# Kernel tuning notes

Hardware: AMD Instinct MI355X
Metric: run time of the kernel (lower is better)

Reference implementation:

```python
import jax, jax.numpy as jnp
import numpy as np

N_NODES = 50000
N_EDGES = 25000  # hyperedges
NNZ = 400000     # incidence pairs


def _segment_mean(x, idx, num_segments):
    s = jax.ops.segment_sum(x, idx, num_segments=num_segments)
    cnt = jax.ops.segment_sum(jnp.ones((x.shape[0], 1), x.dtype), idx, num_segments=num_segments)
    return s / jnp.maximum(cnt, 1.0)


def _unigcn_conv(X, W, vertex, edges, degE, degV):
    # X: [N, Cin] -> [N, Cout]
    X = X @ W                                   # linear (no bias)
    Xve = X[vertex]                             # gather per incidence [nnz, C]
    Xe = _segment_mean(Xve, edges, N_EDGES)     # first_aggregate='mean' over hyperedges
    Xe = Xe * degE                              # [M,1] scale
    Xev = Xe[edges]                             # gather back [nnz, C]
    Xv = jax.ops.segment_sum(Xev, vertex, num_segments=N_NODES)
    return Xv * degV                            # [N,1] scale


def setup_inputs() -> dict:
    key = jax.random.key(0)
    ks = jax.random.split(key, 8)
    nfeat, nhid_total, nclass = 512, 512, 40
    def glorot(k, fan_in, fan_out):
        std = np.sqrt(6.0 / (fan_in + fan_out))
        return jax.random.uniform(k, (fan_in, fan_out), jnp.float32, -std, std)
    return {
        "X": jax.random.normal(ks[0], (N_NODES, nfeat), jnp.float32),
        "vertex": jax.random.randint(ks[1], (NNZ,), 0, N_NODES, jnp.int32),
        "edges": jax.random.randint(ks[2], (NNZ,), 0, N_EDGES, jnp.int32),
        "W1": glorot(ks[3], nfeat, nhid_total),
        "W2": glorot(ks[4], nhid_total, nhid_total),
        "Wout": glorot(ks[5], nhid_total, nclass),
        "degE": jax.random.uniform(ks[6], (N_EDGES, 1), jnp.float32, 0.1, 1.0),
        "degV": jax.random.uniform(ks[7], (N_NODES, 1), jnp.float32, 0.1, 1.0),
    }


def reference(X, vertex, edges, W1, W2, Wout, degE, degV):
    # dropout layers are identity at eval (rates = 0)
    X = jax.nn.relu(_unigcn_conv(X, W1, vertex, edges, degE, degV))
    X = jax.nn.relu(_unigcn_conv(X, W2, vertex, edges, degE, degV))
    X = _unigcn_conv(X, Wout, vertex, edges, degE, degV)
    return jax.nn.log_softmax(X, axis=1)
```

## Files before the change

### kernel.cpp

```cpp
#include <hip/hip_runtime.h>

#define N_NODES 50000
#define N_EDGES_C 25000
#define NNZ_C 400000
#define SCHUNK 2048

typedef __bf16 bf16;
typedef __bf16 bf16x8 __attribute__((ext_vector_type(8)));
typedef __bf16 bf16x4 __attribute__((ext_vector_type(4)));
typedef float f32x4 __attribute__((ext_vector_type(4)));

typedef __attribute__((address_space(1))) const void as1_cvoid;
typedef __attribute__((address_space(3))) void as3_void;

__device__ __forceinline__ void gload_lds16(const bf16* g, bf16* l) {
  __builtin_amdgcn_global_load_lds((as1_cvoid*)g, (as3_void*)l, 16, 0, 0);
}

__global__ void hist_kernel(const int* __restrict__ vtx, const int* __restrict__ edg,
                            int* __restrict__ cntV, int* __restrict__ cntE, int nnz) {
  int i = blockIdx.x * blockDim.x + threadIdx.x;
  if (i < nnz) {
    atomicAdd(&cntV[vtx[i]], 1);
    atomicAdd(&cntE[edg[i]], 1);
  }
}

__global__ void scan_part(const int* __restrict__ cnt, int* __restrict__ part, int n) {
  __shared__ int red[256];
  const int b = blockIdx.x, t = threadIdx.x;
  const int base = b * SCHUNK + t * 8;
  int s = 0;
#pragma unroll
  for (int q = 0; q < 8; ++q) {
    int i = base + q;
    if (i < n) s += cnt[i];
  }
  red[t] = s;
  __syncthreads();
  for (int d = 128; d > 0; d >>= 1) {
    if (t < d) red[t] += red[t + d];
    __syncthreads();
  }
  if (t == 0) part[b] = red[0];
}

__global__ void scan_mid(int* __restrict__ part, int* __restrict__ off, int nparts, int n) {
  const int lane = threadIdx.x;
  int orig = (lane < nparts) ? part[lane] : 0;
  int v = orig;
  for (int o = 1; o < 64; o <<= 1) {
    int x = __shfl_up(v, o);
    if (lane >= o) v += x;
  }
  if (lane < nparts) part[lane] = v - orig;
  if (lane == 63) off[n] = v;
}

__global__ void scan_final(const int* __restrict__ cnt, const int* __restrict__ part,
                           int* __restrict__ off, int n) {
  __shared__ int tsum[256];
  const int b = blockIdx.x, t = threadIdx.x;
  const int base = b * SCHUNK + t * 8;
  int loc[8];
  int s = 0;
#pragma unroll
  for (int q = 0; q < 8; ++q) {
    int i = base + q;
    loc[q] = (i < n) ? cnt[i] : 0;
    s += loc[q];
  }
  tsum[t] = s;
  __syncthreads();
  for (int d = 1; d < 256; d <<= 1) {
    int x = (t >= d) ? tsum[t - d] : 0;
    __syncthreads();
    tsum[t] += x;
    __syncthreads();
  }
  int run = part[b] + ((t > 0) ? tsum[t - 1] : 0);
#pragma unroll
  for (int q = 0; q < 8; ++q) {
    int i = base + q;
    if (i < n) off[i] = run;
    run += loc[q];
  }
}

__global__ void scatter_kernel(const int* __restrict__ vtx, const int* __restrict__ edg,
                               const int* __restrict__ eoff, const int* __restrict__ voff,
                               int* __restrict__ curE, int* __restrict__ curV,
                               int* __restrict__ evtx, int* __restrict__ vedg, int nnz) {
  int i = blockIdx.x * blockDim.x + threadIdx.x;
  if (i < nnz) {
    int e = edg[i], v = vtx[i];
    int p = atomicAdd(&curE[e], 1);
    evtx[eoff[e] + p] = v;
    int q = atomicAdd(&curV[v], 1);
    vedg[voff[v] + q] = e;
  }
}

__global__ void convert_f2b(const float* __restrict__ in, bf16* __restrict__ out, size_t n) {
  size_t i = ((size_t)blockIdx.x * blockDim.x + threadIdx.x) * 4;
  if (i >= n) return;
  float4 v = *(const float4*)(in + i);
  bf16x4 o;
  o[0] = (bf16)v.x; o[1] = (bf16)v.y; o[2] = (bf16)v.z; o[3] = (bf16)v.w;
  *(bf16x4*)(out + i) = o;
}

__global__ void transpose_w(const float* __restrict__ W, bf16* __restrict__ Wt,
                            int K, int N, int NtRows) {
  int idx = blockIdx.x * blockDim.x + threadIdx.x;
  int total = NtRows * K;
  if (idx >= total) return;
  int n = idx / K;
  int k = idx - n * K;
  Wt[idx] = (n < N) ? (bf16)W[(size_t)k * N + n] : (bf16)0.0f;
}

template <int BF16OUT>
__global__ __launch_bounds__(256) void gemm_bf16_kernel(
    const bf16* __restrict__ A, const bf16* __restrict__ B,
    float* __restrict__ Cf, bf16* __restrict__ Cb, int M, int K, int ldC, int Nstore) {
  __shared__ bf16 Al[2][128][64];
  __shared__ bf16 Bl[2][128][64];
  const int t = threadIdx.x;
  const int m0 = blockIdx.x * 128;
  const int n0 = blockIdx.y * 128;
  const int w = t >> 6, lane = t & 63;
  const int wr = w >> 1, wc = w & 1;
  const int lr = lane & 15;
  const int ls = lane >> 4;

  f32x4 acc[4][4];
#pragma unroll
  for (int m = 0; m < 4; ++m)
#pragma unroll
    for (int n = 0; n < 4; ++n) acc[m][n] = (f32x4){0.f, 0.f, 0.f, 0.f};

  const int srow8 = lane >> 3;
  const int scol = ((lane & 7) ^ srow8) << 3;

  const bf16* Abase = A + (size_t)m0 * K;
  const bf16* Bbase = B + (size_t)n0 * K;

#define STAGE(tile, bsel)                                                        \
  {                                                                              \
    const int kk_ = (tile) * 64;                                                 \
    _Pragma("unroll")                                                            \
    for (int q = 0; q < 4; ++q) {                                                \
      const int row = w * 32 + q * 8 + srow8;                                    \
      gload_lds16(Abase + (size_t)row * K + kk_ + scol, &Al[bsel][w*32+q*8][0]); \
      gload_lds16(Bbase + (size_t)row * K + kk_ + scol, &Bl[bsel][w*32+q*8][0]); \
    }                                                                            \
  }

  const int NT = K >> 6;
  STAGE(0, 0);
  for (int tt = 0; tt < NT; ++tt) {
    const int cur = tt & 1;
    if (tt + 1 < NT) {
      STAGE(tt + 1, cur ^ 1);
      asm volatile("s_waitcnt vmcnt(8)" ::: "memory");
    } else {
      asm volatile("s_waitcnt vmcnt(0)" ::: "memory");
    }
    __builtin_amdgcn_s_barrier();
    __builtin_amdgcn_s_setprio(1);
#pragma unroll
    for (int ks = 0; ks < 2; ++ks) {
      bf16x8 af[4], bfr[4];
#pragma unroll
      for (int m = 0; m < 4; ++m) {
        const int R = wr * 64 + m * 16 + lr;
        af[m] = *(const bf16x8*)(&Al[cur][R][((ks * 4 + ls) ^ (lr & 7)) << 3]);
      }
#pragma unroll
      for (int n = 0; n < 4; ++n) {
        const int R = wc * 64 + n * 16 + lr;
        bfr[n] = *(const bf16x8*)(&Bl[cur][R][((ks * 4 + ls) ^ (lr & 7)) << 3]);
      }
#pragma unroll
      for (int m = 0; m < 4; ++m)
#pragma unroll
        for (int n = 0; n < 4; ++n)
          acc[m][n] = __builtin_amdgcn_mfma_f32_16x16x32_bf16(af[m], bfr[n], acc[m][n], 0, 0, 0);
    }
    __builtin_amdgcn_s_setprio(0);
    __builtin_amdgcn_s_barrier();
  }
#undef STAGE

  const int cr = (lane >> 4) << 2;
  const int cc = lane & 15;
#pragma unroll
  for (int m = 0; m < 4; ++m) {
#pragma unroll
    for (int n = 0; n < 4; ++n) {
      int gc = n0 + wc * 64 + n * 16 + cc;
      if (gc >= Nstore) continue;
#pragma unroll
      for (int i = 0; i < 4; ++i) {
        int gr = m0 + wr * 64 + m * 16 + cr + i;
        if (gr < M) {
          if (BF16OUT) Cb[(size_t)gr * ldC + gc] = (bf16)acc[m][n][i];
          else         Cf[(size_t)gr * ldC + gc] = acc[m][n][i];
        }
      }
    }
  }
}

__global__ __launch_bounds__(256) void edge_agg_w(
    const bf16* __restrict__ Y, const int* __restrict__ eoff, const int* __restrict__ evtx,
    const float* __restrict__ degE, bf16* __restrict__ Xe, int nE) {
  const int wv = (blockIdx.x * 256 + threadIdx.x) >> 6;
  if (wv >= nE) return;
  const int lane = threadIdx.x & 63;
  const int beg = eoff[wv], end = eoff[wv + 1];
  const int cnt = end - beg;
  const float scale = (cnt > 0) ? degE[wv] / (float)cnt : 0.f;
  float acc[8] = {0.f, 0.f, 0.f, 0.f, 0.f, 0.f, 0.f, 0.f};
  for (int base = beg; base < end; base += 64) {
    const int nb = min(64, end - base);
    int myidx = (lane < nb) ? evtx[base + lane] : 0;
    int j = 0;
    for (; j + 1 < nb; j += 2) {
      const int i0 = __shfl(myidx, j);
      const int i1 = __shfl(myidx, j + 1);
      bf16x8 v0 = *(const bf16x8*)(Y + (size_t)i0 * 512 + lane * 8);
      bf16x8 v1 = *(const bf16x8*)(Y + (size_t)i1 * 512 + lane * 8);
#pragma unroll
      for (int q = 0; q < 8; ++q) acc[q] += (float)v0[q] + (float)v1[q];
    }
    if (j < nb) {
      const int i0 = __shfl(myidx, j);
      bf16x8 v0 = *(const bf16x8*)(Y + (size_t)i0 * 512 + lane * 8);
#pragma unroll
      for (int q = 0; q < 8; ++q) acc[q] += (float)v0[q];
    }
  }
  bf16x8 o;
#pragma unroll
  for (int q = 0; q < 8; ++q) o[q] = (bf16)(acc[q] * scale);
  *(bf16x8*)(Xe + (size_t)wv * 512 + lane * 8) = o;
}

__global__ __launch_bounds__(256) void vtx_agg_w(
    const bf16* __restrict__ Xe, const int* __restrict__ voff, const int* __restrict__ vedg,
    const float* __restrict__ degV, bf16* __restrict__ outB, int nV) {
  const int wv = (blockIdx.x * 256 + threadIdx.x) >> 6;
  if (wv >= nV) return;
  const int lane = threadIdx.x & 63;
  const int beg = voff[wv], end = voff[wv + 1];
  const float dv = degV[wv];
  float acc[8] = {0.f, 0.f, 0.f, 0.f, 0.f, 0.f, 0.f, 0.f};
  for (int base = beg; base < end; base += 64) {
    const int nb = min(64, end - base);
    int myidx = (lane < nb) ? vedg[base + lane] : 0;
    int j = 0;
    for (; j + 1 < nb; j += 2) {
      const int i0 = __shfl(myidx, j);
      const int i1 = __shfl(myidx, j + 1);
      bf16x8 v0 = *(const bf16x8*)(Xe + (size_t)i0 * 512 + lane * 8);
      bf16x8 v1 = *(const bf16x8*)(Xe + (size_t)i1 * 512 + lane * 8);
#pragma unroll
      for (int q = 0; q < 8; ++q) acc[q] += (float)v0[q] + (float)v1[q];
    }
    if (j < nb) {
      const int i0 = __shfl(myidx, j);
      bf16x8 v0 = *(const bf16x8*)(Xe + (size_t)i0 * 512 + lane * 8);
#pragma unroll
      for (int q = 0; q < 8; ++q) acc[q] += (float)v0[q];
    }
  }
  bf16x8 o;
#pragma unroll
  for (int q = 0; q < 8; ++q) o[q] = (bf16)fmaxf(acc[q] * dv, 0.f);
  *(bf16x8*)(outB + (size_t)wv * 512 + lane * 8) = o;
}

__global__ __launch_bounds__(256) void edge_agg40_w(
    const float* __restrict__ Y, const int* __restrict__ eoff, const int* __restrict__ evtx,
    const float* __restrict__ degE, float* __restrict__ Xe, int nE) {
  const int wv = (blockIdx.x * 256 + threadIdx.x) >> 6;
  if (wv >= nE) return;
  const int lane = threadIdx.x & 63;
  const int beg = eoff[wv], end = eoff[wv + 1];
  const int cnt = end - beg;
  const float scale = (cnt > 0) ? degE[wv] / (float)cnt : 0.f;
  float a0 = 0.f;
  for (int base = beg; base < end; base += 64) {
    const int nb = min(64, end - base);
    int myidx = (lane < nb) ? evtx[base + lane] : 0;
    int j = 0;
    for (; j + 3 < nb; j += 4) {
      const int i0 = __shfl(myidx, j);
      const int i1 = __shfl(myidx, j + 1);
      const int i2 = __shfl(myidx, j + 2);
      const int i3 = __shfl(myidx, j + 3);
      if (lane < 40) {
        float x0 = Y[(size_t)i0 * 40 + lane];
        float x1 = Y[(size_t)i1 * 40 + lane];
        float x2 = Y[(size_t)i2 * 40 + lane];
        float x3 = Y[(size_t)i3 * 40 + lane];
        a0 += (x0 + x1) + (x2 + x3);
      }
    }
    for (; j < nb; ++j) {
      const int i0 = __shfl(myidx, j);
      if (lane < 40) a0 += Y[(size_t)i0 * 40 + lane];
    }
  }
  if (lane < 40) Xe[(size_t)wv * 40 + lane] = a0 * scale;
}

__global__ __launch_bounds__(256) void vtx_agg_lsm(
    const float* __restrict__ Xe, const int* __restrict__ voff, const int* __restrict__ vedg,
    const float* __restrict__ degV, float* __restrict__ out, int nV) {
  const int wv = (blockIdx.x * 256 + threadIdx.x) >> 6;
  if (wv >= nV) return;
  const int lane = threadIdx.x & 63;
  const int beg = voff[wv], end = voff[wv + 1];
  const float dv = degV[wv];
  float a0 = 0.f;
  for (int base = beg; base < end; base += 64) {
    const int nb = min(64, end - base);
    int myidx = (lane < nb) ? vedg[base + lane] : 0;
    int j = 0;
    for (; j + 3 < nb; j += 4) {
      const int i0 = __shfl(myidx, j);
      const int i1 = __shfl(myidx, j + 1);
      const int i2 = __shfl(myidx, j + 2);
      const int i3 = __shfl(myidx, j + 3);
      if (lane < 40) {
        float x0 = Xe[(size_t)i0 * 40 + lane];
        float x1 = Xe[(size_t)i1 * 40 + lane];
        float x2 = Xe[(size_t)i2 * 40 + lane];
        float x3 = Xe[(size_t)i3 * 40 + lane];
        a0 += (x0 + x1) + (x2 + x3);
      }
    }
    for (; j < nb; ++j) {
      const int i0 = __shfl(myidx, j);
      if (lane < 40) a0 += Xe[(size_t)i0 * 40 + lane];
    }
  }
  a0 *= dv;
  float val = (lane < 40) ? a0 : -3.4e38f;
  float m = val;
#pragma unroll
  for (int o = 32; o > 0; o >>= 1) m = fmaxf(m, __shfl_xor(m, o));
  float ex = (lane < 40) ? expf(val - m) : 0.f;
  float s = ex;
#pragma unroll
  for (int o = 32; o > 0; o >>= 1) s += __shfl_xor(s, o);
  float ls = logf(s);
  if (lane < 40) out[(size_t)wv * 40 + lane] = val - m - ls;
}

extern "C" void kernel_launch(void* const* d_in, const int* in_sizes, int n_in,
                              void* d_out, int out_size, void* d_ws, size_t ws_size,
                              hipStream_t stream) {
  (void)in_sizes; (void)n_in; (void)out_size; (void)ws_size;
  const float* X = (const float*)d_in[0];
  const int* vertex = (const int*)d_in[1];
  const int* edges = (const int*)d_in[2];
  const float* W1 = (const float*)d_in[3];
  const float* W2 = (const float*)d_in[4];
  const float* Wout = (const float*)d_in[5];
  const float* degE = (const float*)d_in[6];
  const float* degV = (const float*)d_in[7];
  float* out = (float*)d_out;

  char* ws = (char*)d_ws;
  size_t off = 0;
  auto alloc = [&](size_t bytes) -> void* {
    void* p = ws + off;
    off += (bytes + 255) & ~(size_t)255;
    return p;
  };
  bf16* Xb  = (bf16*)alloc((size_t)N_NODES * 512 * sizeof(bf16));
  bf16* Yb  = (bf16*)alloc((size_t)N_NODES * 512 * sizeof(bf16));
  bf16* XeB = (bf16*)alloc((size_t)N_EDGES_C * 512 * sizeof(bf16));
  float* Y40  = (float*)alloc((size_t)N_NODES * 40 * sizeof(float));
  float* Xe40 = (float*)alloc((size_t)N_EDGES_C * 40 * sizeof(float));
  bf16* Wt  = (bf16*)alloc((size_t)512 * 512 * sizeof(bf16));
  int* eoff = (int*)alloc((N_EDGES_C + 1) * sizeof(int));
  int* voff = (int*)alloc((N_NODES + 1) * sizeof(int));
  int* evtx = (int*)alloc((size_t)NNZ_C * sizeof(int));
  int* vedg = (int*)alloc((size_t)NNZ_C * sizeof(int));
  int* cntE = (int*)alloc(N_EDGES_C * sizeof(int));
  int* cntV = (int*)alloc(N_NODES * sizeof(int));
  int* curE = (int*)alloc(N_EDGES_C * sizeof(int));
  int* curV = (int*)alloc(N_NODES * sizeof(int));
  int* partE = (int*)alloc(64 * sizeof(int));
  int* partV = (int*)alloc(64 * sizeof(int));

  hipMemsetAsync(cntE, 0, N_EDGES_C * sizeof(int), stream);
  hipMemsetAsync(cntV, 0, N_NODES * sizeof(int), stream);
  hipMemsetAsync(curE, 0, N_EDGES_C * sizeof(int), stream);
  hipMemsetAsync(curV, 0, N_NODES * sizeof(int), stream);

  hist_kernel<<<(NNZ_C + 255) / 256, 256, 0, stream>>>(vertex, edges, cntV, cntE, NNZ_C);

  const int nbE = (N_EDGES_C + SCHUNK - 1) / SCHUNK;
  const int nbV = (N_NODES + SCHUNK - 1) / SCHUNK;
  scan_part<<<nbE, 256, 0, stream>>>(cntE, partE, N_EDGES_C);
  scan_mid<<<1, 64, 0, stream>>>(partE, eoff, nbE, N_EDGES_C);
  scan_final<<<nbE, 256, 0, stream>>>(cntE, partE, eoff, N_EDGES_C);
  scan_part<<<nbV, 256, 0, stream>>>(cntV, partV, N_NODES);
  scan_mid<<<1, 64, 0, stream>>>(partV, voff, nbV, N_NODES);
  scan_final<<<nbV, 256, 0, stream>>>(cntV, partV, voff, N_NODES);

  scatter_kernel<<<(NNZ_C + 255) / 256, 256, 0, stream>>>(vertex, edges, eoff, voff,
                                                          curE, curV, evtx, vedg, NNZ_C);

  convert_f2b<<<(N_NODES * 512 / 4 + 255) / 256, 256, 0, stream>>>(X, Xb, (size_t)N_NODES * 512);

  const int MB = (N_NODES + 127) / 128;

  transpose_w<<<(512 * 512 + 255) / 256, 256, 0, stream>>>(W1, Wt, 512, 512, 512);
  {
    dim3 g(MB, 4);
    gemm_bf16_kernel<1><<<g, 256, 0, stream>>>(Xb, Wt, nullptr, Yb, N_NODES, 512, 512, 512);
  }
  edge_agg_w<<<(N_EDGES_C + 3) / 4, 256, 0, stream>>>(Yb, eoff, evtx, degE, XeB, N_EDGES_C);
  vtx_agg_w<<<(N_NODES + 3) / 4, 256, 0, stream>>>(XeB, voff, vedg, degV, Xb, N_NODES);

  transpose_w<<<(512 * 512 + 255) / 256, 256, 0, stream>>>(W2, Wt, 512, 512, 512);
  {
    dim3 g(MB, 4);
    gemm_bf16_kernel<1><<<g, 256, 0, stream>>>(Xb, Wt, nullptr, Yb, N_NODES, 512, 512, 512);
  }
  edge_agg_w<<<(N_EDGES_C + 3) / 4, 256, 0, stream>>>(Yb, eoff, evtx, degE, XeB, N_EDGES_C);
  vtx_agg_w<<<(N_NODES + 3) / 4, 256, 0, stream>>>(XeB, voff, vedg, degV, Xb, N_NODES);

  transpose_w<<<(128 * 512 + 255) / 256, 256, 0, stream>>>(Wout, Wt, 512, 40, 128);
  {
    dim3 g(MB, 1);
    gemm_bf16_kernel<0><<<g, 256, 0, stream>>>(Xb, Wt, Y40, nullptr, N_NODES, 512, 40, 40);
  }
  edge_agg40_w<<<(N_EDGES_C + 3) / 4, 256, 0, stream>>>(Y40, eoff, evtx, degE, Xe40, N_EDGES_C);
  vtx_agg_lsm<<<(N_NODES + 3) / 4, 256, 0, stream>>>(Xe40, voff, vedg, degV, out, N_NODES);
}
```

Measured before the change: 543.7 us.

## Merge prep and scan launches, swap GEMM grid order, store final layer in bf16

Fuses the weight transposes and the X conversion into one prep kernel, and merges the paired E/V scan kernels and the four memsets into single launches to cut launch count. The GEMM grid is reordered so the four N-tiles of the same M rows run next to each other, which should improve L2 reuse of A. The 40-wide final layer now stores its intermediates in bf16, halving gather traffic at some precision cost.

```diff
diff --git a/kernel.cpp b/kernel.cpp
--- a/kernel.cpp
+++ b/kernel.cpp
@@ -26,9 +26,15 @@
   }
 }
 
-__global__ void scan_part(const int* __restrict__ cnt, int* __restrict__ part, int n) {
+__global__ void scan_part2(const int* __restrict__ cntE, const int* __restrict__ cntV,
+                           int* __restrict__ partE, int* __restrict__ partV,
+                           int nbE) {
   __shared__ int red[256];
-  const int b = blockIdx.x, t = threadIdx.x;
+  const int t = threadIdx.x;
+  const int isV = (blockIdx.x >= nbE);
+  const int b = isV ? (blockIdx.x - nbE) : blockIdx.x;
+  const int* cnt = isV ? cntV : cntE;
+  const int n = isV ? N_NODES : N_EDGES_C;
   const int base = b * SCHUNK + t * 8;
   int s = 0;
 #pragma unroll
@@ -42,25 +48,39 @@
     if (t < d) red[t] += red[t + d];
     __syncthreads();
   }
-  if (t == 0) part[b] = red[0];
-}
-
-__global__ void scan_mid(int* __restrict__ part, int* __restrict__ off, int nparts, int n) {
-  const int lane = threadIdx.x;
-  int orig = (lane < nparts) ? part[lane] : 0;
+  if (t == 0) (isV ? partV : partE)[b] = red[0];
+}
+
+__global__ void scan_mid2(int* __restrict__ partE, int* __restrict__ partV,
+                          int* __restrict__ eoff, int* __restrict__ voff,
+                          int nbE, int nbV) {
+  const int wv = threadIdx.x >> 6;
+  const int lane = threadIdx.x & 63;
+  int* part = wv ? partV : partE;
+  int* off = wv ? voff : eoff;
+  const int np = wv ? nbV : nbE;
+  const int n = wv ? N_NODES : N_EDGES_C;
+  int orig = (lane < np) ? part[lane] : 0;
   int v = orig;
   for (int o = 1; o < 64; o <<= 1) {
     int x = __shfl_up(v, o);
     if (lane >= o) v += x;
   }
-  if (lane < nparts) part[lane] = v - orig;
+  if (lane < np) part[lane] = v - orig;
   if (lane == 63) off[n] = v;
 }
 
-__global__ void scan_final(const int* __restrict__ cnt, const int* __restrict__ part,
-                           int* __restrict__ off, int n) {
+__global__ void scan_final2(const int* __restrict__ cntE, const int* __restrict__ cntV,
+                            const int* __restrict__ partE, const int* __restrict__ partV,
+                            int* __restrict__ eoff, int* __restrict__ voff, int nbE) {
   __shared__ int tsum[256];
-  const int b = blockIdx.x, t = threadIdx.x;
+  const int t = threadIdx.x;
+  const int isV = (blockIdx.x >= nbE);
+  const int b = isV ? (blockIdx.x - nbE) : blockIdx.x;
+  const int* cnt = isV ? cntV : cntE;
+  const int* part = isV ? partV : partE;
+  int* off = isV ? voff : eoff;
+  const int n = isV ? N_NODES : N_EDGES_C;
   const int base = b * SCHUNK + t * 8;
   int loc[8];
   int s = 0;
@@ -101,23 +121,33 @@
   }
 }
 
-__global__ void convert_f2b(const float* __restrict__ in, bf16* __restrict__ out, size_t n) {
-  size_t i = ((size_t)blockIdx.x * blockDim.x + threadIdx.x) * 4;
-  if (i >= n) return;
-  float4 v = *(const float4*)(in + i);
-  bf16x4 o;
-  o[0] = (bf16)v.x; o[1] = (bf16)v.y; o[2] = (bf16)v.z; o[3] = (bf16)v.w;
-  *(bf16x4*)(out + i) = o;
-}
-
-__global__ void transpose_w(const float* __restrict__ W, bf16* __restrict__ Wt,
-                            int K, int N, int NtRows) {
-  int idx = blockIdx.x * blockDim.x + threadIdx.x;
-  int total = NtRows * K;
-  if (idx >= total) return;
-  int n = idx / K;
-  int k = idx - n * K;
-  Wt[idx] = (n < N) ? (bf16)W[(size_t)k * N + n] : (bf16)0.0f;
+__global__ void prep_conv(const float* __restrict__ W1, const float* __restrict__ W2,
+                          const float* __restrict__ Wout, const float* __restrict__ X,
+                          bf16* __restrict__ Wt1, bf16* __restrict__ Wt2,
+                          bf16* __restrict__ Wt3, bf16* __restrict__ Xb) {
+  const int b = blockIdx.x;
+  const int t = threadIdx.x;
+  if (b < 1024) {
+    int idx = b * 256 + t;
+    int n = idx >> 9, k = idx & 511;
+    Wt1[idx] = (bf16)W1[(size_t)k * 512 + n];
+  } else if (b < 2048) {
+    int idx = (b - 1024) * 256 + t;
+    int n = idx >> 9, k = idx & 511;
+    Wt2[idx] = (bf16)W2[(size_t)k * 512 + n];
+  } else if (b < 2304) {
+    int idx = (b - 2048) * 256 + t;
+    int n = idx >> 9, k = idx & 511;
+    Wt3[idx] = (n < 40) ? (bf16)Wout[(size_t)k * 40 + n] : (bf16)0.0f;
+  } else {
+    size_t i = ((size_t)(b - 2304) * 256 + t) * 8;
+    float4 v0 = *(const float4*)(X + i);
+    float4 v1 = *(const float4*)(X + i + 4);
+    bf16x8 o;
+    o[0] = (bf16)v0.x; o[1] = (bf16)v0.y; o[2] = (bf16)v0.z; o[3] = (bf16)v0.w;
+    o[4] = (bf16)v1.x; o[5] = (bf16)v1.y; o[6] = (bf16)v1.z; o[7] = (bf16)v1.w;
+    *(bf16x8*)(Xb + i) = o;
+  }
 }
 
 template <int BF16OUT>
@@ -127,8 +157,8 @@
   __shared__ bf16 Al[2][128][64];
   __shared__ bf16 Bl[2][128][64];
   const int t = threadIdx.x;
-  const int m0 = blockIdx.x * 128;
-  const int n0 = blockIdx.y * 128;
+  const int n0 = blockIdx.x * 128;
+  const int m0 = blockIdx.y * 128;
   const int w = t >> 6, lane = t & 63;
   const int wr = w >> 1, wc = w & 1;
   const int lr = lane & 15;
@@ -283,8 +313,8 @@
 }
 
 __global__ __launch_bounds__(256) void edge_agg40_w(
-    const float* __restrict__ Y, const int* __restrict__ eoff, const int* __restrict__ evtx,
-    const float* __restrict__ degE, float* __restrict__ Xe, int nE) {
+    const bf16* __restrict__ Y, const int* __restrict__ eoff, const int* __restrict__ evtx,
+    const float* __restrict__ degE, bf16* __restrict__ Xe, int nE) {
   const int wv = (blockIdx.x * 256 + threadIdx.x) >> 6;
   if (wv >= nE) return;
   const int lane = threadIdx.x & 63;
@@ -302,23 +332,23 @@
       const int i2 = __shfl(myidx, j + 2);
       const int i3 = __shfl(myidx, j + 3);
       if (lane < 40) {
-        float x0 = Y[(size_t)i0 * 40 + lane];
-        float x1 = Y[(size_t)i1 * 40 + lane];
-        float x2 = Y[(size_t)i2 * 40 + lane];
-        float x3 = Y[(size_t)i3 * 40 + lane];
+        float x0 = (float)Y[(size_t)i0 * 40 + lane];
+        float x1 = (float)Y[(size_t)i1 * 40 + lane];
+        float x2 = (float)Y[(size_t)i2 * 40 + lane];
+        float x3 = (float)Y[(size_t)i3 * 40 + lane];
         a0 += (x0 + x1) + (x2 + x3);
       }
     }
     for (; j < nb; ++j) {
       const int i0 = __shfl(myidx, j);
-      if (lane < 40) a0 += Y[(size_t)i0 * 40 + lane];
-    }
-  }
-  if (lane < 40) Xe[(size_t)wv * 40 + lane] = a0 * scale;
+      if (lane < 40) a0 += (float)Y[(size_t)i0 * 40 + lane];
+    }
+  }
+  if (lane < 40) Xe[(size_t)wv * 40 + lane] = (bf16)(a0 * scale);
 }
 
 __global__ __launch_bounds__(256) void vtx_agg_lsm(
-    const float* __restrict__ Xe, const int* __restrict__ voff, const int* __restrict__ vedg,
+    const bf16* __restrict__ Xe, const int* __restrict__ voff, const int* __restrict__ vedg,
     const float* __restrict__ degV, float* __restrict__ out, int nV) {
   const int wv = (blockIdx.x * 256 + threadIdx.x) >> 6;
   if (wv >= nV) return;
@@ -336,16 +366,16 @@
       const int i2 = __shfl(myidx, j + 2);
       const int i3 = __shfl(myidx, j + 3);
       if (lane < 40) {
-        float x0 = Xe[(size_t)i0 * 40 + lane];
-        float x1 = Xe[(size_t)i1 * 40 + lane];
-        float x2 = Xe[(size_t)i2 * 40 + lane];
-        float x3 = Xe[(size_t)i3 * 40 + lane];
+        float x0 = (float)Xe[(size_t)i0 * 40 + lane];
+        float x1 = (float)Xe[(size_t)i1 * 40 + lane];
+        float x2 = (float)Xe[(size_t)i2 * 40 + lane];
+        float x3 = (float)Xe[(size_t)i3 * 40 + lane];
         a0 += (x0 + x1) + (x2 + x3);
       }
     }
     for (; j < nb; ++j) {
       const int i0 = __shfl(myidx, j);
-      if (lane < 40) a0 += Xe[(size_t)i0 * 40 + lane];
+      if (lane < 40) a0 += (float)Xe[(size_t)i0 * 40 + lane];
     }
   }
   a0 *= dv;
@@ -385,64 +415,58 @@
   bf16* Xb  = (bf16*)alloc((size_t)N_NODES * 512 * sizeof(bf16));
   bf16* Yb  = (bf16*)alloc((size_t)N_NODES * 512 * sizeof(bf16));
   bf16* XeB = (bf16*)alloc((size_t)N_EDGES_C * 512 * sizeof(bf16));
-  float* Y40  = (float*)alloc((size_t)N_NODES * 40 * sizeof(float));
-  float* Xe40 = (float*)alloc((size_t)N_EDGES_C * 40 * sizeof(float));
-  bf16* Wt  = (bf16*)alloc((size_t)512 * 512 * sizeof(bf16));
+  bf16* Y40b  = (bf16*)alloc((size_t)N_NODES * 40 * sizeof(bf16));
+  bf16* Xe40b = (bf16*)alloc((size_t)N_EDGES_C * 40 * sizeof(bf16));
+  bf16* Wt1 = (bf16*)alloc((size_t)512 * 512 * sizeof(bf16));
+  bf16* Wt2 = (bf16*)alloc((size_t)512 * 512 * sizeof(bf16));
+  bf16* Wt3 = (bf16*)alloc((size_t)128 * 512 * sizeof(bf16));
   int* eoff = (int*)alloc((N_EDGES_C + 1) * sizeof(int));
   int* voff = (int*)alloc((N_NODES + 1) * sizeof(int));
   int* evtx = (int*)alloc((size_t)NNZ_C * sizeof(int));
   int* vedg = (int*)alloc((size_t)NNZ_C * sizeof(int));
-  int* cntE = (int*)alloc(N_EDGES_C * sizeof(int));
-  int* cntV = (int*)alloc(N_NODES * sizeof(int));
-  int* curE = (int*)alloc(N_EDGES_C * sizeof(int));
-  int* curV = (int*)alloc(N_NODES * sizeof(int));
+  int* cnts = (int*)alloc((size_t)(2 * (N_EDGES_C + N_NODES)) * sizeof(int));
+  int* cntE = cnts;
+  int* cntV = cnts + N_EDGES_C;
+  int* curE = cnts + N_EDGES_C + N_NODES;
+  int* curV = cnts + 2 * N_EDGES_C + N_NODES;
   int* partE = (int*)alloc(64 * sizeof(int));
   int* partV = (int*)alloc(64 * sizeof(int));
 
-  hipMemsetAsync(cntE, 0, N_EDGES_C * sizeof(int), stream);
-  hipMemsetAsync(cntV, 0, N_NODES * sizeof(int), stream);
-  hipMemsetAsync(curE, 0, N_EDGES_C * sizeof(int), stream);
-  hipMemsetAsync(curV, 0, N_NODES * sizeof(int), stream);
+  hipMemsetAsync(cnts, 0, (size_t)(2 * (N_EDGES_C + N_NODES)) * sizeof(int), stream);
+
+  prep_conv<<<2304 + 12500, 256, 0, stream>>>(W1, W2, Wout, X, Wt1, Wt2, Wt3, Xb);
 
   hist_kernel<<<(NNZ_C + 255) / 256, 256, 0, stream>>>(vertex, edges, cntV, cntE, NNZ_C);
 
   const int nbE = (N_EDGES_C + SCHUNK - 1) / SCHUNK;
   const int nbV = (N_NODES + SCHUNK - 1) / SCHUNK;
-  scan_part<<<nbE, 256, 0, stream>>>(cntE, partE, N_EDGES_C);
-  scan_mid<<<1, 64, 0, stream>>>(partE, eoff, nbE, N_EDGES_C);
-  scan_final<<<nbE, 256, 0, stream>>>(cntE, partE, eoff, N_EDGES_C);
-  scan_part<<<nbV, 256, 0, stream>>>(cntV, partV, N_NODES);
-  scan_mid<<<1, 64, 0, stream>>>(partV, voff, nbV, N_NODES);
-  scan_final<<<nbV, 256, 0, stream>>>(cntV, partV, voff, N_NODES);
+  scan_part2<<<nbE + nbV, 256, 0, stream>>>(cntE, cntV, partE, partV, nbE);
+  scan_mid2<<<1, 128, 0, stream>>>(partE, partV, eoff, voff, nbE, nbV);
+  scan_final2<<<nbE + nbV, 256, 0, stream>>>(cntE, cntV, partE, partV, eoff, voff, nbE);
 
   scatter_kernel<<<(NNZ_C + 255) / 256, 256, 0, stream>>>(vertex, edges, eoff, voff,
                                                           curE, curV, evtx, vedg, NNZ_C);
 
-  convert_f2b<<<(N_NODES * 512 / 4 + 255) / 256, 256, 0, stream>>>(X, Xb, (size_t)N_NODES * 512);
-
   const int MB = (N_NODES + 127) / 128;
 
-  transpose_w<<<(512 * 512 + 255) / 256, 256, 0, stream>>>(W1, Wt, 512, 512, 512);
   {
-    dim3 g(MB, 4);
-    gemm_bf16_kernel<1><<<g, 256, 0, stream>>>(Xb, Wt, nullptr, Yb, N_NODES, 512, 512, 512);
+    dim3 g(4, MB);
+    gemm_bf16_kernel<1><<<g, 256, 0, stream>>>(Xb, Wt1, nullptr, Yb, N_NODES, 512, 512, 512);
   }
   edge_agg_w<<<(N_EDGES_C + 3) / 4, 256, 0, stream>>>(Yb, eoff, evtx, degE, XeB, N_EDGES_C);
   vtx_agg_w<<<(N_NODES + 3) / 4, 256, 0, stream>>>(XeB, voff, vedg, degV, Xb, N_NODES);
 
-  transpose_w<<<(512 * 512 + 255) / 256, 256, 0, stream>>>(W2, Wt, 512, 512, 512);
   {
-    dim3 g(MB, 4);
-    gemm_bf16_kernel<1><<<g, 256, 0, stream>>>(Xb, Wt, nullptr, Yb, N_NODES, 512, 512, 512);
+    dim3 g(4, MB);
+    gemm_bf16_kernel<1><<<g, 256, 0, stream>>>(Xb, Wt2, nullptr, Yb, N_NODES, 512, 512, 512);
   }
   edge_agg_w<<<(N_EDGES_C + 3) / 4, 256, 0, stream>>>(Yb, eoff, evtx, degE, XeB, N_EDGES_C);
   vtx_agg_w<<<(N_NODES + 3) / 4, 256, 0, stream>>>(XeB, voff, vedg, degV, Xb, N_NODES);
 
-  transpose_w<<<(128 * 512 + 255) / 256, 256, 0, stream>>>(Wout, Wt, 512, 40, 128);
   {
-    dim3 g(MB, 1);
-    gemm_bf16_kernel<0><<<g, 256, 0, stream>>>(Xb, Wt, Y40, nullptr, N_NODES, 512, 40, 40);
-  }
-  edge_agg40_w<<<(N_EDGES_C + 3) / 4, 256, 0, stream>>>(Y40, eoff, evtx, degE, Xe40, N_EDGES_C);
-  vtx_agg_lsm<<<(N_NODES + 3) / 4, 256, 0, stream>>>(Xe40, voff, vedg, degV, out, N_NODES);
-}
+    dim3 g(1, MB);
+    gemm_bf16_kernel<1><<<g, 256, 0, stream>>>(Xb, Wt3, nullptr, Y40b, N_NODES, 512, 40, 40);
+  }
+  edge_agg40_w<<<(N_EDGES_C + 3) / 4, 256, 0, stream>>>(Y40b, eoff, evtx, degE, Xe40b, N_EDGES_C);
+  vtx_agg_lsm<<<(N_NODES + 3) / 4, 256, 0, stream>>>(Xe40b, voff, vedg, degV, out, N_NODES);
+}
```

After: 511.7 us. 5.9% less time.
